# Optimization experiments

Measured on AMD Instinct MI355X. Metric: run time of the kernel, lower is better.

Reference implementation:

```python
import jax, jax.numpy as jnp
import numpy as np

BN_EPS = 1e-5
K = 3  # number of nearest neighbors for interpolation


def setup_inputs() -> dict:
    key = jax.random.key(0)
    ks = jax.random.split(key, 16)
    B, N1, N2 = 8, 8192, 2048
    C2, C1, H = 256, 128, 256  # in_channels, skip_channels, out_channels
    total_in = C2 + C1
    inp = {
        "xyz1": jax.random.normal(ks[0], (B, 3, N1), dtype=jnp.float32),
        "xyz2": jax.random.normal(ks[1], (B, 3, N2), dtype=jnp.float32),
        "features1": jax.random.normal(ks[2], (B, C1, N1), dtype=jnp.float32),
        "features2": jax.random.normal(ks[3], (B, C2, N2), dtype=jnp.float32),
        # SharedMLP([total_in, H, H]): two 1x1 Conv1d + BatchNorm1d (eval mode) + ReLU
        "w1": jax.random.normal(ks[4], (H, total_in), dtype=jnp.float32) * 0.05,
        "b1": jax.random.normal(ks[5], (H,), dtype=jnp.float32) * 0.01,
        "g1": 1.0 + 0.1 * jax.random.normal(ks[6], (H,), dtype=jnp.float32),
        "be1": 0.1 * jax.random.normal(ks[7], (H,), dtype=jnp.float32),
        "m1": 0.1 * jax.random.normal(ks[8], (H,), dtype=jnp.float32),
        "v1": 0.5 + jax.random.uniform(ks[9], (H,), dtype=jnp.float32),
        "w2": jax.random.normal(ks[10], (H, H), dtype=jnp.float32) * 0.05,
        "b2": jax.random.normal(ks[11], (H,), dtype=jnp.float32) * 0.01,
        "g2": 1.0 + 0.1 * jax.random.normal(ks[12], (H,), dtype=jnp.float32),
        "be2": 0.1 * jax.random.normal(ks[13], (H,), dtype=jnp.float32),
        "m2": 0.1 * jax.random.normal(ks[14], (H,), dtype=jnp.float32),
        "v2": 0.5 + jax.random.uniform(ks[15], (H,), dtype=jnp.float32),
    }
    return inp


def _conv_bn_relu(x, w, b, g, be, m, v):
    # x: [B, Cin, N], w: [Cout, Cin] (1x1 conv), BN in eval mode
    y = jnp.einsum("oc,bcn->bon", w, x) + b[None, :, None]
    y = (y - m[None, :, None]) * (g / jnp.sqrt(v + BN_EPS))[None, :, None] + be[None, :, None]
    return jax.nn.relu(y)


def reference(xyz1, xyz2, features1, features2,
              w1, b1, g1, be1, m1, v1,
              w2, b2, g2, be2, m2, v2):
    # --- squared pairwise distances [B, N1, N2] ---
    x1 = jnp.transpose(xyz1, (0, 2, 1))  # [B, N1, 3]
    x2 = jnp.transpose(xyz2, (0, 2, 1))  # [B, N2, 3]
    sq = (jnp.sum(x1 * x1, axis=-1, keepdims=True)
          + jnp.sum(x2 * x2, axis=-1)[:, None, :]
          - 2.0 * jnp.einsum("bnd,bmd->bnm", x1, x2))
    # --- k=3 nearest neighbors (smallest sq distances) ---
    neg_d, idx = jax.lax.top_k(-sq, K)          # [B, N1, K]
    dist = jnp.maximum(-neg_d, 1e-10)
    weight = 1.0 / dist
    weight = weight / jnp.sum(weight, axis=-1, keepdims=True)  # [B, N1, K]
    # --- gather neighbor features and inverse-distance interpolate ---
    feat2_t = jnp.transpose(features2, (0, 2, 1))              # [B, N2, C2]
    neighbor = jax.vmap(lambda f, i: f[i])(feat2_t, idx)       # [B, N1, K, C2]
    interp = jnp.einsum("bnkc,bnk->bnc", neighbor, weight)     # [B, N1, C2]
    interp = jnp.transpose(interp, (0, 2, 1))                  # [B, C2, N1]
    # --- concat skip features and shared MLP ---
    x = jnp.concatenate([interp, features1], axis=1)           # [B, C2+C1, N1]
    x = _conv_bn_relu(x, w1, b1, g1, be1, m1, v1)
    x = _conv_bn_relu(x, w2, b2, g2, be2, m2, v2)
    return x
```

## Files before the change

kernel.cpp:

```cpp
#include <hip/hip_runtime.h>
#include <hip/hip_bf16.h>

typedef unsigned short u16;
typedef __attribute__((ext_vector_type(4))) float f32x4;
typedef __attribute__((ext_vector_type(8))) short short8;

#define BN_EPS 1e-5f

__device__ __forceinline__ u16 f2b(float x) {
  union { float f; unsigned int u; } v; v.f = x;
  unsigned int r = (v.u + 0x7FFFu + ((v.u >> 16) & 1u)) >> 16;
  return (u16)r;
}
__device__ __forceinline__ float b2f(u16 u) {
  union { unsigned int u; float f; } v; v.u = ((unsigned int)u) << 16;
  return v.f;
}

__global__ void prep_kernel(const float* __restrict__ w1, const float* __restrict__ b1,
                            const float* __restrict__ g1, const float* __restrict__ be1,
                            const float* __restrict__ m1, const float* __restrict__ v1,
                            const float* __restrict__ w2, const float* __restrict__ b2,
                            const float* __restrict__ g2, const float* __restrict__ be2,
                            const float* __restrict__ m2, const float* __restrict__ v2,
                            u16* __restrict__ w1b, u16* __restrict__ w2b,
                            float* __restrict__ al1, float* __restrict__ bt1,
                            float* __restrict__ al2, float* __restrict__ bt2) {
  int t = threadIdx.x;
  int blk = blockIdx.x;
  if (blk < 384) {
    int id = blk * 256 + t;
    unsigned o = (unsigned)id / 384u;
    unsigned c = (unsigned)id % 384u;
    w1b[(c >> 5) * 8192 + o * 32 + (c & 31)] = f2b(w1[id]);
  } else if (blk < 640) {
    int j = (blk - 384) * 256 + t;
    unsigned o = (unsigned)j >> 8;
    unsigned c = (unsigned)j & 255u;
    w2b[(c >> 5) * 8192 + o * 32 + (c & 31)] = f2b(w2[j]);
  } else if (blk == 640) {
    float a = g1[t] / sqrtf(v1[t] + BN_EPS);
    al1[t] = a;
    bt1[t] = (b1[t] - m1[t]) * a + be1[t];
  } else {
    float a = g2[t] / sqrtf(v2[t] + BN_EPS);
    al2[t] = a;
    bt2[t] = (b2[t] - m2[t]) * a + be2[t];
  }
}

__global__ void transpose_f2_kernel(const float* __restrict__ f2, u16* __restrict__ f2t) {
  __shared__ float tile[32][33];
  int t = threadIdx.x;
  int tx = t & 31, ty = t >> 5;
  int b = blockIdx.z;
  int n2t = blockIdx.x * 32, ct = blockIdx.y * 32;
#pragma unroll
  for (int i = 0; i < 4; ++i) {
    int c = ct + ty + i * 8;
    tile[ty + i * 8][tx] = f2[((size_t)b * 256 + c) * 2048 + n2t + tx];
  }
  __syncthreads();
#pragma unroll
  for (int i = 0; i < 4; ++i) {
    int n2 = n2t + ty + i * 8;
    f2t[((size_t)b * 2048 + n2) * 256 + ct + tx] = f2b(tile[tx][ty + i * 8]);
  }
}

__global__ __launch_bounds__(256) void knn_interp_kernel(
    const float* __restrict__ xyz1, const float* __restrict__ xyz2,
    const float* __restrict__ f1, const u16* __restrict__ f2t,
    u16* __restrict__ xb) {
  union Lds {
    struct { float4 pts[2048]; float md[256 * 3]; int mi[256 * 3]; } a;
    float f1t[128 * 65];
  };
  __shared__ Lds lds;
  __shared__ float wts[64 * 3];
  __shared__ int idxs[64 * 3];

  int t = threadIdx.x;
  int b = blockIdx.x >> 7;
  int n1_0 = (blockIdx.x & 127) * 64;
  int panel = blockIdx.x;

  const float* x2 = xyz2 + b * 3 * 2048;
  for (int j = t; j < 2048; j += 256) {
    float cx = x2[j], cy = x2[2048 + j], cz = x2[4096 + j];
    float nsq = (cx * cx + cy * cy) + cz * cz;
    lds.a.pts[j] = make_float4(cx, cy, cz, nsq);
  }
  __syncthreads();

  {
    int p = t & 63, s = t >> 6;
    int n1 = n1_0 + p;
    const float* x1 = xyz1 + b * 3 * 8192;
    float bx = x1[n1], by = x1[8192 + n1], bz = x1[16384 + n1];
    float n1sq = (bx * bx + by * by) + bz * bz;
    float nx = -2.f * bx, ny = -2.f * by, nz = -2.f * bz;
    float d0 = 3.4e38f, d1 = 3.4e38f, d2 = 3.4e38f;
    int i0 = 0, i1 = 0, i2 = 0;
    int jb = s * 512;
#pragma unroll 4
    for (int jj = 0; jj < 512; ++jj) {
      float4 c = lds.a.pts[jb + jj];
      float sq = fmaf(nx, c.x, fmaf(ny, c.y, fmaf(nz, c.z, n1sq + c.w)));
      int j = jb + jj;
      bool c0 = sq < d0, c1 = sq < d1, c2 = sq < d2;
      d2 = c1 ? d1 : (c2 ? sq : d2);  i2 = c1 ? i1 : (c2 ? j : i2);
      d1 = c0 ? d0 : (c1 ? sq : d1); i1 = c0 ? i0 : (c1 ? j : i1);
      d0 = c0 ? sq : d0;             i0 = c0 ? j : i0;
    }
    lds.a.md[t * 3 + 0] = d0; lds.a.md[t * 3 + 1] = d1; lds.a.md[t * 3 + 2] = d2;
    lds.a.mi[t * 3 + 0] = i0; lds.a.mi[t * 3 + 1] = i1; lds.a.mi[t * 3 + 2] = i2;
  }
  __syncthreads();
  if (t < 64) {
    float d0 = 3.4e38f, d1 = 3.4e38f, d2 = 3.4e38f;
    int i0 = 0, i1 = 0, i2 = 0;
#pragma unroll
    for (int s = 0; s < 4; ++s) {
#pragma unroll
      for (int k = 0; k < 3; ++k) {
        float d = lds.a.md[(s * 64 + t) * 3 + k];
        int i = lds.a.mi[(s * 64 + t) * 3 + k];
        bool c0 = d < d0, c1 = d < d1, c2 = d < d2;
        i2 = c1 ? i1 : (c2 ? i : i2);
        i1 = c0 ? i0 : (c1 ? i : i1);
        i0 = c0 ? i : i0;
        d2 = c1 ? d1 : (c2 ? d : d2);
        d1 = c0 ? d0 : (c1 ? d : d1);
        d0 = c0 ? d : d0;
      }
    }
    float e0 = fmaxf(d0, 1e-10f), e1 = fmaxf(d1, 1e-10f), e2 = fmaxf(d2, 1e-10f);
    float w0 = 1.0f / e0, w1 = 1.0f / e1, w2 = 1.0f / e2;
    float sm = (w0 + w1) + w2;
    wts[t * 3 + 0] = w0 / sm; wts[t * 3 + 1] = w1 / sm; wts[t * 3 + 2] = w2 / sm;
    idxs[t * 3 + 0] = i0 * 256; idxs[t * 3 + 1] = i1 * 256; idxs[t * 3 + 2] = i2 * 256;
  }
  __syncthreads();

  {
    const u16* f2tb = f2t + (size_t)b * 2048 * 256;
    size_t xbase = (size_t)panel * 24576 + (size_t)((t >> 5) * 2048) + (t & 31);
#pragma unroll 4
    for (int p = 0; p < 64; ++p) {
      int j0 = idxs[p * 3 + 0], j1 = idxs[p * 3 + 1], j2 = idxs[p * 3 + 2];
      float w0 = wts[p * 3 + 0], w1 = wts[p * 3 + 1], w2 = wts[p * 3 + 2];
      float v = (w0 * b2f(f2tb[j0 + t]) + w1 * b2f(f2tb[j1 + t]))
                + w2 * b2f(f2tb[j2 + t]);
      xb[xbase + p * 32] = f2b(v);
    }
  }
  __syncthreads();

  {
    const float* f1b = f1 + (size_t)b * 128 * 8192 + n1_0;
    for (int it = 0; it < 32; ++it) {
      int c = it * 4 + (t >> 6);
      int n = t & 63;
      lds.f1t[c * 65 + n] = f1b[(size_t)c * 8192 + n];
    }
    __syncthreads();
    for (int it = 0; it < 32; ++it) {
      int v = it * 256 + t;
      int c = v & 127, p = v >> 7;
      float val = lds.f1t[c * 65 + p];
      xb[(size_t)panel * 24576 + (size_t)(8 + (c >> 5)) * 2048 + p * 32 + (c & 31)] = f2b(val);
    }
  }
}

__global__ __launch_bounds__(256) void gemm_fused_kernel(
    const u16* __restrict__ xin, const u16* __restrict__ w1b,
    const u16* __restrict__ w2b,
    const float* __restrict__ al1, const float* __restrict__ bt1,
    const float* __restrict__ al2, const float* __restrict__ bt2,
    float* __restrict__ fout) {
  __shared__ u16 y1t[8 * 64 * 40];
  int t = threadIdx.x;
  int panel = blockIdx.x;
  int w = t >> 6, lane = t & 63, l15 = lane & 15, quad = lane >> 4;

  f32x4 acc[4][4];
#pragma unroll
  for (int m = 0; m < 4; ++m)
#pragma unroll
    for (int n = 0; n < 4; ++n)
      acc[m][n] = (f32x4){0.f, 0.f, 0.f, 0.f};

  {
    const u16* aw = w1b + (size_t)(w * 64 + l15) * 32 + quad * 8;
    const u16* bx = xin + (size_t)panel * (12 * 2048) + (size_t)l15 * 32 + quad * 8;
    short8 af[2][4], bf[2][4];
#pragma unroll
    for (int m = 0; m < 4; ++m)
      af[0][m] = *(const short8*)(aw + m * 512);
#pragma unroll
    for (int n = 0; n < 4; ++n)
      bf[0][n] = *(const short8*)(bx + n * 512);
#pragma unroll
    for (int kt = 0; kt < 12; ++kt) {
      int cur = kt & 1, nxt = cur ^ 1;
      if (kt < 11) {
#pragma unroll
        for (int m = 0; m < 4; ++m)
          af[nxt][m] = *(const short8*)(aw + (kt + 1) * 8192 + m * 512);
#pragma unroll
        for (int n = 0; n < 4; ++n)
          bf[nxt][n] = *(const short8*)(bx + (kt + 1) * 2048 + n * 512);
      }
#pragma unroll
      for (int m = 0; m < 4; ++m)
#pragma unroll
        for (int n = 0; n < 4; ++n)
          acc[m][n] = __builtin_amdgcn_mfma_f32_16x16x32_bf16(af[cur][m], bf[cur][n], acc[m][n], 0, 0, 0);
    }
  }

  {
    float al[4][4], bt[4][4];
#pragma unroll
    for (int m = 0; m < 4; ++m)
#pragma unroll
      for (int r = 0; r < 4; ++r) {
        int o = w * 64 + m * 16 + quad * 4 + r;
        al[m][r] = al1[o];
        bt[m][r] = bt1[o];
      }
#pragma unroll
    for (int m = 0; m < 4; ++m) {
      int kt2 = w * 2 + (m >> 1);
      int osub = (m & 1) * 16 + quad * 4;
#pragma unroll
      for (int n = 0; n < 4; ++n) {
        int col = n * 16 + l15;
        ushort4 pk;
        pk.x = f2b(fmaxf(fmaf(al[m][0], acc[m][n][0], bt[m][0]), 0.f));
        pk.y = f2b(fmaxf(fmaf(al[m][1], acc[m][n][1], bt[m][1]), 0.f));
        pk.z = f2b(fmaxf(fmaf(al[m][2], acc[m][n][2], bt[m][2]), 0.f));
        pk.w = f2b(fmaxf(fmaf(al[m][3], acc[m][n][3], bt[m][3]), 0.f));
        *(ushort4*)&y1t[(kt2 * 64 + col) * 40 + osub] = pk;
      }
    }
  }
  __syncthreads();

#pragma unroll
  for (int m = 0; m < 4; ++m)
#pragma unroll
    for (int n = 0; n < 4; ++n)
      acc[m][n] = (f32x4){0.f, 0.f, 0.f, 0.f};
  {
    const u16* aw = w2b + (size_t)(w * 64 + l15) * 32 + quad * 8;
    short8 af[2][4];
#pragma unroll
    for (int m = 0; m < 4; ++m)
      af[0][m] = *(const short8*)(aw + m * 512);
#pragma unroll
    for (int kt = 0; kt < 8; ++kt) {
      int cur = kt & 1, nxt = cur ^ 1;
      if (kt < 7) {
#pragma unroll
        for (int m = 0; m < 4; ++m)
          af[nxt][m] = *(const short8*)(aw + (kt + 1) * 8192 + m * 512);
      }
      short8 bf[4];
#pragma unroll
      for (int n = 0; n < 4; ++n)
        bf[n] = *(const short8*)&y1t[(kt * 64 + n * 16 + l15) * 40 + quad * 8];
#pragma unroll
      for (int m = 0; m < 4; ++m)
#pragma unroll
        for (int n = 0; n < 4; ++n)
          acc[m][n] = __builtin_amdgcn_mfma_f32_16x16x32_bf16(af[cur][m], bf[n], acc[m][n], 0, 0, 0);
    }
  }

  {
    float al[4][4], bt[4][4];
#pragma unroll
    for (int m = 0; m < 4; ++m)
#pragma unroll
      for (int r = 0; r < 4; ++r) {
        int o = w * 64 + m * 16 + quad * 4 + r;
        al[m][r] = al2[o];
        bt[m][r] = bt2[o];
      }
    int bb = panel >> 7;
    int n1base = (panel & 127) * 64;
#pragma unroll
    for (int m = 0; m < 4; ++m)
#pragma unroll
      for (int n = 0; n < 4; ++n) {
        int col = n * 16 + l15;
#pragma unroll
        for (int r = 0; r < 4; ++r) {
          int o = w * 64 + m * 16 + quad * 4 + r;
          float vv = fmaxf(fmaf(al[m][r], acc[m][n][r], bt[m][r]), 0.f);
          fout[(size_t)(bb * 256 + o) * 8192 + n1base + col] = vv;
        }
      }
  }
}

extern "C" void kernel_launch(void* const* d_in, const int* in_sizes, int n_in,
                              void* d_out, int out_size, void* d_ws, size_t ws_size,
                              hipStream_t stream) {
  const float* xyz1 = (const float*)d_in[0];
  const float* xyz2 = (const float*)d_in[1];
  const float* f1   = (const float*)d_in[2];
  const float* f2   = (const float*)d_in[3];
  const float* w1   = (const float*)d_in[4];
  const float* b1   = (const float*)d_in[5];
  const float* g1   = (const float*)d_in[6];
  const float* be1  = (const float*)d_in[7];
  const float* m1   = (const float*)d_in[8];
  const float* v1   = (const float*)d_in[9];
  const float* w2   = (const float*)d_in[10];
  const float* b2   = (const float*)d_in[11];
  const float* g2   = (const float*)d_in[12];
  const float* be2  = (const float*)d_in[13];
  const float* m2   = (const float*)d_in[14];
  const float* v2   = (const float*)d_in[15];

  char* ws = (char*)d_ws;
  u16* xb   = (u16*)(ws);
  u16* f2t  = (u16*)(ws + 50331648);
  u16* w1b  = (u16*)(ws + 83886080);
  u16* w2b  = (u16*)(ws + 84082688);
  float* al1 = (float*)(ws + 84213760);
  float* bt1 = (float*)(ws + 84214784);
  float* al2 = (float*)(ws + 84215808);
  float* bt2 = (float*)(ws + 84216832);
  float* out = (float*)d_out;

  prep_kernel<<<642, 256, 0, stream>>>(w1, b1, g1, be1, m1, v1,
                                       w2, b2, g2, be2, m2, v2,
                                       w1b, w2b, al1, bt1, al2, bt2);
  transpose_f2_kernel<<<dim3(64, 8, 8), 256, 0, stream>>>(f2, f2t);
  knn_interp_kernel<<<1024, 256, 0, stream>>>(xyz1, xyz2, f1, f2t, xb);
  gemm_fused_kernel<<<1024, 256, 0, stream>>>(xb, w1b, w2b, al1, bt1, al2, bt2, out);
}
```

Baseline: 233.5 us.

## Split KNN selection into separate single-wave kernel with warp-uniform early skip

Separates the fused KNN+interpolation kernel into a 64-thread selection kernel that scans all 2048 candidates per point and an interpolation kernel that reads weights and indices from workspace. The selection loop now skips the top-3 insertion update when no lane in the wave beats its current third-best distance, which avoids most of the select work once the lists settle. The smaller LDS footprint and block size are meant to raise occupancy, and the 4-way partial-merge step is gone. In exchange it adds a kernel launch, a global round trip for weights and indices, and a serial 2048-long loop per thread.

```diff
diff --git a/kernel.cpp b/kernel.cpp
--- a/kernel.cpp
+++ b/kernel.cpp
@@ -68,78 +68,72 @@
   }
 }
 
-__global__ __launch_bounds__(256) void knn_interp_kernel(
+__global__ __launch_bounds__(64) void knn_select_kernel(
     const float* __restrict__ xyz1, const float* __restrict__ xyz2,
+    float* __restrict__ wi, int* __restrict__ ii) {
+  __shared__ float4 pts[2048];
+  int t = threadIdx.x;
+  int panel = blockIdx.x;
+  int b = panel >> 7;
+  int n1 = (panel & 127) * 64 + t;
+
+  const float* x2 = xyz2 + b * 3 * 2048;
+#pragma unroll 4
+  for (int j0 = 0; j0 < 2048; j0 += 64) {
+    int j = j0 + t;
+    float cx = x2[j], cy = x2[2048 + j], cz = x2[4096 + j];
+    pts[j] = make_float4(cx, cy, cz, (cx * cx + cy * cy) + cz * cz);
+  }
+  __syncthreads();
+
+  const float* x1 = xyz1 + b * 3 * 8192;
+  float bx = x1[n1], by = x1[8192 + n1], bz = x1[16384 + n1];
+  float n1sq = (bx * bx + by * by) + bz * bz;
+  float nx = -2.f * bx, ny = -2.f * by, nz = -2.f * bz;
+
+  float d0 = 3.4e38f, d1 = 3.4e38f, d2 = 3.4e38f;
+  int i0 = 0, i1 = 0, i2 = 0;
+#pragma unroll 4
+  for (int j = 0; j < 2048; ++j) {
+    float4 c = pts[j];
+    float sq = fmaf(nx, c.x, fmaf(ny, c.y, fmaf(nz, c.z, n1sq + c.w)));
+    bool upd = sq < d2;
+    if (__any(upd)) {
+      bool c0 = upd && (sq < d0);
+      bool c1 = upd && (sq < d1);
+      i2 = c1 ? i1 : (upd ? j : i2);
+      d2 = c1 ? d1 : (upd ? sq : d2);
+      i1 = c0 ? i0 : (c1 ? j : i1);
+      d1 = c0 ? d0 : (c1 ? sq : d1);
+      i0 = c0 ? j : i0;
+      d0 = c0 ? sq : d0;
+    }
+  }
+
+  float e0 = fmaxf(d0, 1e-10f), e1 = fmaxf(d1, 1e-10f), e2 = fmaxf(d2, 1e-10f);
+  float w0 = 1.0f / e0, w1 = 1.0f / e1, w2 = 1.0f / e2;
+  float sm = (w0 + w1) + w2;
+  float* wp = wi + panel * 192 + t * 3;
+  int* ip = ii + panel * 192 + t * 3;
+  wp[0] = w0 / sm; wp[1] = w1 / sm; wp[2] = w2 / sm;
+  ip[0] = i0 * 256; ip[1] = i1 * 256; ip[2] = i2 * 256;
+}
+
+__global__ __launch_bounds__(256) void interp_kernel(
     const float* __restrict__ f1, const u16* __restrict__ f2t,
+    const float* __restrict__ wi, const int* __restrict__ ii,
     u16* __restrict__ xb) {
-  union Lds {
-    struct { float4 pts[2048]; float md[256 * 3]; int mi[256 * 3]; } a;
-    float f1t[128 * 65];
-  };
-  __shared__ Lds lds;
-  __shared__ float wts[64 * 3];
-  __shared__ int idxs[64 * 3];
-
-  int t = threadIdx.x;
-  int b = blockIdx.x >> 7;
-  int n1_0 = (blockIdx.x & 127) * 64;
+  __shared__ float f1t[128 * 65];
+  __shared__ float wts[192];
+  __shared__ int idxs[192];
+  int t = threadIdx.x;
   int panel = blockIdx.x;
-
-  const float* x2 = xyz2 + b * 3 * 2048;
-  for (int j = t; j < 2048; j += 256) {
-    float cx = x2[j], cy = x2[2048 + j], cz = x2[4096 + j];
-    float nsq = (cx * cx + cy * cy) + cz * cz;
-    lds.a.pts[j] = make_float4(cx, cy, cz, nsq);
-  }
-  __syncthreads();
-
-  {
-    int p = t & 63, s = t >> 6;
-    int n1 = n1_0 + p;
-    const float* x1 = xyz1 + b * 3 * 8192;
-    float bx = x1[n1], by = x1[8192 + n1], bz = x1[16384 + n1];
-    float n1sq = (bx * bx + by * by) + bz * bz;
-    float nx = -2.f * bx, ny = -2.f * by, nz = -2.f * bz;
-    float d0 = 3.4e38f, d1 = 3.4e38f, d2 = 3.4e38f;
-    int i0 = 0, i1 = 0, i2 = 0;
-    int jb = s * 512;
-#pragma unroll 4
-    for (int jj = 0; jj < 512; ++jj) {
-      float4 c = lds.a.pts[jb + jj];
-      float sq = fmaf(nx, c.x, fmaf(ny, c.y, fmaf(nz, c.z, n1sq + c.w)));
-      int j = jb + jj;
-      bool c0 = sq < d0, c1 = sq < d1, c2 = sq < d2;
-      d2 = c1 ? d1 : (c2 ? sq : d2);  i2 = c1 ? i1 : (c2 ? j : i2);
-      d1 = c0 ? d0 : (c1 ? sq : d1); i1 = c0 ? i0 : (c1 ? j : i1);
-      d0 = c0 ? sq : d0;             i0 = c0 ? j : i0;
-    }
-    lds.a.md[t * 3 + 0] = d0; lds.a.md[t * 3 + 1] = d1; lds.a.md[t * 3 + 2] = d2;
-    lds.a.mi[t * 3 + 0] = i0; lds.a.mi[t * 3 + 1] = i1; lds.a.mi[t * 3 + 2] = i2;
-  }
-  __syncthreads();
-  if (t < 64) {
-    float d0 = 3.4e38f, d1 = 3.4e38f, d2 = 3.4e38f;
-    int i0 = 0, i1 = 0, i2 = 0;
-#pragma unroll
-    for (int s = 0; s < 4; ++s) {
-#pragma unroll
-      for (int k = 0; k < 3; ++k) {
-        float d = lds.a.md[(s * 64 + t) * 3 + k];
-        int i = lds.a.mi[(s * 64 + t) * 3 + k];
-        bool c0 = d < d0, c1 = d < d1, c2 = d < d2;
-        i2 = c1 ? i1 : (c2 ? i : i2);
-        i1 = c0 ? i0 : (c1 ? i : i1);
-        i0 = c0 ? i : i0;
-        d2 = c1 ? d1 : (c2 ? d : d2);
-        d1 = c0 ? d0 : (c1 ? d : d1);
-        d0 = c0 ? d : d0;
-      }
-    }
-    float e0 = fmaxf(d0, 1e-10f), e1 = fmaxf(d1, 1e-10f), e2 = fmaxf(d2, 1e-10f);
-    float w0 = 1.0f / e0, w1 = 1.0f / e1, w2 = 1.0f / e2;
-    float sm = (w0 + w1) + w2;
-    wts[t * 3 + 0] = w0 / sm; wts[t * 3 + 1] = w1 / sm; wts[t * 3 + 2] = w2 / sm;
-    idxs[t * 3 + 0] = i0 * 256; idxs[t * 3 + 1] = i1 * 256; idxs[t * 3 + 2] = i2 * 256;
+  int b = panel >> 7;
+  int n1_0 = (panel & 127) * 64;
+
+  if (t < 192) {
+    wts[t] = wi[panel * 192 + t];
+    idxs[t] = ii[panel * 192 + t];
   }
   __syncthreads();
 
@@ -155,20 +149,19 @@
       xb[xbase + p * 32] = f2b(v);
     }
   }
-  __syncthreads();
 
   {
     const float* f1b = f1 + (size_t)b * 128 * 8192 + n1_0;
     for (int it = 0; it < 32; ++it) {
       int c = it * 4 + (t >> 6);
       int n = t & 63;
-      lds.f1t[c * 65 + n] = f1b[(size_t)c * 8192 + n];
+      f1t[c * 65 + n] = f1b[(size_t)c * 8192 + n];
     }
     __syncthreads();
     for (int it = 0; it < 32; ++it) {
       int v = it * 256 + t;
       int c = v & 127, p = v >> 7;
-      float val = lds.f1t[c * 65 + p];
+      float val = f1t[c * 65 + p];
       xb[(size_t)panel * 24576 + (size_t)(8 + (c >> 5)) * 2048 + p * 32 + (c & 31)] = f2b(val);
     }
   }
@@ -330,6 +323,8 @@
   char* ws = (char*)d_ws;
   u16* xb   = (u16*)(ws);
   u16* f2t  = (u16*)(ws + 50331648);
+  float* wi = (float*)(ws + 58720256);
+  int* ii   = (int*)(ws + 59506688);
   u16* w1b  = (u16*)(ws + 83886080);
   u16* w2b  = (u16*)(ws + 84082688);
   float* al1 = (float*)(ws + 84213760);
@@ -342,6 +337,7 @@
                                        w2, b2, g2, be2, m2, v2,
                                        w1b, w2b, al1, bt1, al2, bt2);
   transpose_f2_kernel<<<dim3(64, 8, 8), 256, 0, stream>>>(f2, f2t);
-  knn_interp_kernel<<<1024, 256, 0, stream>>>(xyz1, xyz2, f1, f2t, xb);
+  knn_select_kernel<<<1024, 64, 0, stream>>>(xyz1, xyz2, wi, ii);
+  interp_kernel<<<1024, 256, 0, stream>>>(f1, f2t, wi, ii, xb);
   gemm_fused_kernel<<<1024, 256, 0, stream>>>(xb, w1b, w2b, al1, bt1, al2, bt2, out);
 }
```

Result: slower. 337.6 us (+44.6%).
